# Kernel tuning notes

Measured on AMD Instinct MI355X. Metric: run time of the kernel, lower is better.

Reference implementation:

```python
import jax, jax.numpy as jnp
import numpy as np

DIM = 1024
HEADS = 16
DIM_HEAD = 64
INNER = HEADS * DIM_HEAD  # 1024
B, N = 4, 1024
SCALE = DIM_HEAD ** -0.5


def _layernorm(t, g, b, eps=1e-5):
    mu = jnp.mean(t, axis=-1, keepdims=True)
    var = jnp.var(t, axis=-1, keepdims=True)
    return (t - mu) * jax.lax.rsqrt(var + eps) * g + b


def setup_inputs() -> dict:
    key = jax.random.key(0)
    ks = jax.random.split(key, 8)
    return {
        "x": jax.random.normal(ks[0], (B, N, DIM), dtype=jnp.float32),
        "y": jax.random.normal(ks[1], (B, N, DIM), dtype=jnp.float32),
        "gx": jnp.ones((DIM,), jnp.float32),
        "bx": jnp.zeros((DIM,), jnp.float32),
        "gy": jnp.ones((DIM,), jnp.float32),
        "by": jnp.zeros((DIM,), jnp.float32),
        "Wqkv_x": jax.random.normal(ks[2], (DIM, 3 * INNER), jnp.float32) * 0.02,
        "Wqkv_y": jax.random.normal(ks[3], (DIM, 3 * INNER), jnp.float32) * 0.02,
        "Wout_x": jax.random.normal(ks[4], (INNER, DIM), jnp.float32) * 0.02,
        "bout_x": jnp.zeros((DIM,), jnp.float32),
        "Wout_y": jax.random.normal(ks[5], (INNER, DIM), jnp.float32) * 0.02,
        "bout_y": jnp.zeros((DIM,), jnp.float32),
    }


def _split_heads(t):
    b, n, _ = t.shape
    return t.reshape(b, n, HEADS, DIM_HEAD).transpose(0, 2, 1, 3)  # b h n d


def reference(x, y, gx, bx, gy, by, Wqkv_x, Wqkv_y, Wout_x, bout_x, Wout_y, bout_y):
    xn = _layernorm(x, gx, bx)
    yn = _layernorm(y, gy, by)
    qx, kx, vx = [_split_heads(t) for t in jnp.split(xn @ Wqkv_x, 3, axis=-1)]
    qy, ky, vy = [_split_heads(t) for t in jnp.split(yn @ Wqkv_y, 3, axis=-1)]
    # concat along HEADS dim -> 2h heads; each stream's heads attend within that stream
    q = jnp.concatenate([qx, qy], axis=1)
    k = jnp.concatenate([kx, ky], axis=1)
    v = jnp.concatenate([vx, vy], axis=1)
    dots = jnp.einsum('bhid,bhjd->bhij', q, k) * SCALE  # [B, 2h, N, N]
    attn = jax.nn.softmax(dots, axis=-1)
    out = jnp.einsum('bhij,bhjd->bhid', attn, v)  # [B, 2h, N, d]
    xo = out[:, :HEADS]  # original code uses the x-chunk for BOTH outputs (faithful)
    xo = xo.transpose(0, 2, 1, 3).reshape(xo.shape[0], xo.shape[2], INNER)  # b n (h d)
    out_x = xo @ Wout_x + bout_x
    out_y = xo @ Wout_y + bout_y
    return (out_x, out_y)
```

## Files before the change

### kernel.cpp

```cpp
#include <hip/hip_runtime.h>

typedef __attribute__((ext_vector_type(8))) short s16x8;
typedef __attribute__((ext_vector_type(4))) float f32x4;
typedef unsigned short u16;

#define DEV __device__ __forceinline__

DEV u16 f2bf(float f) {
    unsigned u = __builtin_bit_cast(unsigned, f);
    unsigned r = u + 0x7fffu + ((u >> 16) & 1u);
    return (u16)(r >> 16);
}

DEV float exp2a(float x) {
    float r;
    asm("v_exp_f32 %0, %1" : "=v"(r) : "v"(x));
    return r;
}

DEV unsigned cvtpk(float lo, float hi) {
    unsigned r;
    asm("v_cvt_pk_bf16_f32 %0, %1, %2" : "=v"(r) : "v"(lo), "v"(hi));
    return r;
}

DEV void gload_lds16(const void* g, void* l) {
    __builtin_amdgcn_global_load_lds(
        (const __attribute__((address_space(1))) unsigned int*)g,
        (__attribute__((address_space(3))) unsigned int*)l, 16, 0, 0);
}

DEV f32x4 mfma16(s16x8 a, s16x8 b, f32x4 c) {
    return __builtin_amdgcn_mfma_f32_16x16x32_bf16(a, b, c, 0, 0, 0);
}

template <int N>
DEV void vmwait() {
    asm volatile("s_waitcnt vmcnt(%0)" ::"n"(N) : "memory");
}

__global__ __launch_bounds__(256) void ln_kernel(const float* __restrict__ x,
                                                 const float* __restrict__ g,
                                                 const float* __restrict__ b,
                                                 u16* __restrict__ xn) {
    const int row = blockIdx.x, t = threadIdx.x;
    const float4 v = *(const float4*)(x + (size_t)row * 1024 + t * 4);
    float s1 = v.x + v.y + v.z + v.w;
    float s2 = v.x * v.x + v.y * v.y + v.z * v.z + v.w * v.w;
#pragma unroll
    for (int d = 1; d < 64; d <<= 1) {
        s1 += __shfl_xor(s1, d);
        s2 += __shfl_xor(s2, d);
    }
    __shared__ float red[8];
    if ((t & 63) == 0) { red[(t >> 6) * 2] = s1; red[(t >> 6) * 2 + 1] = s2; }
    __syncthreads();
    s1 = red[0] + red[2] + red[4] + red[6];
    s2 = red[1] + red[3] + red[5] + red[7];
    const float mu = s1 * (1.0f / 1024.0f);
    const float var = s2 * (1.0f / 1024.0f) - mu * mu;
    const float rs = rsqrtf(var + 1e-5f);
    const float4 gv = *(const float4*)(g + t * 4);
    const float4 bv = *(const float4*)(b + t * 4);
    ushort4 o;
    o.x = f2bf((v.x - mu) * rs * gv.x + bv.x);
    o.y = f2bf((v.y - mu) * rs * gv.y + bv.y);
    o.z = f2bf((v.z - mu) * rs * gv.z + bv.z);
    o.w = f2bf((v.w - mu) * rs * gv.w + bv.w);
    *(ushort4*)(xn + (size_t)row * 1024 + t * 4) = o;
}

__global__ __launch_bounds__(256) void transpose_w(const float* __restrict__ src,
                                                   u16* __restrict__ dst, int ld) {
    __shared__ float tile[64][68];
    const int t = threadIdx.x;
    const int n0 = blockIdx.x * 64, k0 = blockIdx.y * 64;
    const int kl = t >> 4, nl = (t & 15) * 4;
#pragma unroll
    for (int p = 0; p < 4; ++p) {
        float4 v = *(const float4*)(src + (size_t)(k0 + kl + p * 16) * ld + n0 + nl);
        tile[kl + p * 16][nl + 0] = v.x;
        tile[kl + p * 16][nl + 1] = v.y;
        tile[kl + p * 16][nl + 2] = v.z;
        tile[kl + p * 16][nl + 3] = v.w;
    }
    __syncthreads();
    const int nl2 = t >> 2, kc = (t & 3) * 16;
    __align__(16) u16 tmp[16];
#pragma unroll
    for (int j = 0; j < 16; ++j) tmp[j] = f2bf(tile[kc + j][nl2]);
    u16* d = dst + (size_t)(n0 + nl2) * 1024 + k0 + kc;
    ((uint4*)d)[0] = ((const uint4*)tmp)[0];
    ((uint4*)d)[1] = ((const uint4*)tmp)[1];
}

__global__ __launch_bounds__(256) void transpose_v(const u16* __restrict__ V,
                                                   u16* __restrict__ Vt) {
    __shared__ u16 tile[64][72];
    const int t = threadIdx.x;
    const int j0 = blockIdx.x * 64;
    const int bh = blockIdx.y;
    const u16* src = V + (size_t)bh * 65536;
    const int jl = t >> 4, dl = (t & 15) * 4;
#pragma unroll
    for (int p = 0; p < 4; ++p) {
        ushort4 v = *(const ushort4*)(src + (size_t)(j0 + jl + p * 16) * 64 + dl);
        *(ushort4*)&tile[jl + p * 16][dl] = v;
    }
    __syncthreads();
    const int dl2 = t >> 2, jc = (t & 3) * 16;
    __align__(16) u16 tmp[16];
#pragma unroll
    for (int j = 0; j < 16; ++j) tmp[j] = tile[jc + j][dl2];
    u16* d = Vt + (size_t)bh * 65536 + (size_t)dl2 * 1024 + j0 + jc;
    ((uint4*)d)[0] = ((const uint4*)tmp)[0];
    ((uint4*)d)[1] = ((const uint4*)tmp)[1];
}

template <int BN, int WM, int EPI>
__global__ __launch_bounds__(512, 2) void gemm8(const u16* __restrict__ A,
                                                const u16* __restrict__ B,
                                                u16* __restrict__ Qb, u16* __restrict__ Kb,
                                                u16* __restrict__ Vb,
                                                const float* __restrict__ bx,
                                                const float* __restrict__ by,
                                                float* __restrict__ out, int NBX) {
    constexpr int BM = 256, WN = 8 / WM;
    constexpr int TM = BM / WM, TN = BN / WN;
    constexpr int MQ = TM / 32, NQ = TN / 32;
    constexpr int HA = TM / 2, HB = TN / 2;
    constexpr int CHA = 1024;
    constexpr int CHB = BN * 4;
    constexpr int GA = 2, GB = CHB / 512;
    constexpr int NI = 8;

    __shared__ __align__(16) u16 As[2 * 2 * CHA * 8];
    __shared__ __align__(16) u16 Bs[2 * 2 * CHB * 8];

    const int tid = threadIdx.x, lane = tid & 63;
    const int wave = tid >> 6;
    const int wm = wave / WN, wn = wave % WN;
    const int lr = lane & 15, cg = lane >> 4;

    const int nwg = NBX * 16;
    const int bid = blockIdx.x;
    const int bid2 = (bid & 7) * (nwg >> 3) + (bid >> 3);
    const int bxi = bid2 % NBX, byi = bid2 / NBX;
    const int m0 = byi * 256, n0 = bxi * BN;

    const u16* __restrict__ Ag = A + (size_t)m0 * 1024;
    const u16* __restrict__ Bg = B + (size_t)n0 * 1024;

    f32x4 acc[2 * MQ][2 * NQ] = {};

#define STG_A(b, h, t)                                                              \
    do {                                                                            \
        _Pragma("unroll") for (int u = 0; u < GA; ++u) {                            \
            const int idx = u * 512 + tid;                                          \
            const int loc = idx >> 3, pp = idx & 7;                                 \
            const int row = (loc & (HA - 1)) | ((h)*HA) | ((loc / HA) * 2 * HA);    \
            gload_lds16(Ag + (size_t)row * 1024 + (t)*64 + ((pp ^ (row & 7)) << 3), \
                        &As[(((b)*2 + (h)) * CHA + idx) * 8]);                      \
        }                                                                           \
    } while (0)
#define STG_B(b, h, t)                                                              \
    do {                                                                            \
        _Pragma("unroll") for (int u = 0; u < GB; ++u) {                            \
            const int idx = u * 512 + tid;                                          \
            const int loc = idx >> 3, pp = idx & 7;                                 \
            const int row = (loc & (HB - 1)) | ((h)*HB) | ((loc / HB) * 2 * HB);    \
            gload_lds16(Bg + (size_t)row * 1024 + (t)*64 + ((pp ^ (row & 7)) << 3), \
                        &Bs[(((b)*2 + (h)) * CHB + idx) * 8]);                      \
        }                                                                           \
    } while (0)

#define LDA(bb, lm, dst)                                                            \
    _Pragma("unroll") for (int mf = 0; mf < MQ; ++mf)                               \
        _Pragma("unroll") for (int ks = 0; ks < 2; ++ks)                            \
            dst[mf][ks] = *(const s16x8*)&As[((((bb)*2 + (lm)) * CHA) +             \
                                              (mf * 16 + lr + wm * HA) * 8 +        \
                                              ((cg + ks * 4) ^ (lr & 7))) * 8];

#define LDB(bb, ln, dst)                                                            \
    _Pragma("unroll") for (int nf = 0; nf < NQ; ++nf)                               \
        _Pragma("unroll") for (int ks = 0; ks < 2; ++ks)                            \
            dst[nf][ks] = *(const s16x8*)&Bs[((((bb)*2 + (ln)) * CHB) +             \
                                              (nf * 16 + lr + wn * HB) * 8 +        \
                                              ((cg + ks * 4) ^ (lr & 7))) * 8];

#define MM(lm, ln, A_, B_)                                                          \
    __builtin_amdgcn_s_setprio(1);                                                  \
    _Pragma("unroll") for (int mf = 0; mf < MQ; ++mf)                               \
        _Pragma("unroll") for (int nf = 0; nf < NQ; ++nf)                           \
            _Pragma("unroll") for (int ks = 0; ks < 2; ++ks)                        \
                acc[(lm)*MQ + mf][(ln)*NQ + nf] = mfma16(                           \
                    A_[mf][ks], B_[nf][ks], acc[(lm)*MQ + mf][(ln)*NQ + nf]);       \
    __builtin_amdgcn_s_setprio(0);

#define BAR() asm volatile("s_barrier" ::: "memory")

    STG_A(0, 0, 0);
    STG_A(0, 1, 0);
    STG_B(0, 0, 0);
    STG_B(0, 1, 0);
    STG_A(1, 0, 1);
    STG_B(1, 0, 1);
    vmwait<GA + GB>();
    BAR();

    s16x8 va[MQ][2];
    s16x8 vb[2][NQ][2];

#pragma unroll 1
    for (int i = 0; i < NI - 1; ++i) {
        const int t1 = 2 * i + 1, t2 = 2 * i + 2, t3 = 2 * i + 3;
        LDA(0, 0, va); LDB(0, 0, vb[0]); STG_A(1, 1, t1); BAR(); MM(0, 0, va, vb[0]);
        LDB(0, 1, vb[1]);                STG_B(1, 1, t1); BAR(); MM(0, 1, va, vb[1]);
        LDA(0, 1, va);                   STG_A(0, 0, t2); BAR(); MM(1, 0, va, vb[0]);
        STG_B(0, 0, t2); vmwait<GA + GB>();               BAR(); MM(1, 1, va, vb[1]);
        LDA(1, 0, va); LDB(1, 0, vb[0]); STG_A(0, 1, t2); BAR(); MM(0, 0, va, vb[0]);
        LDB(1, 1, vb[1]);                STG_B(0, 1, t2); BAR(); MM(0, 1, va, vb[1]);
        LDA(1, 1, va);                   STG_A(1, 0, t3); BAR(); MM(1, 0, va, vb[0]);
        STG_B(1, 0, t3); vmwait<GA + GB>();               BAR(); MM(1, 1, va, vb[1]);
    }
    LDA(0, 0, va); LDB(0, 0, vb[0]); STG_A(1, 1, 15); BAR(); MM(0, 0, va, vb[0]);
    LDB(0, 1, vb[1]);                STG_B(1, 1, 15); BAR(); MM(0, 1, va, vb[1]);
    LDA(0, 1, va);                                    BAR(); MM(1, 0, va, vb[0]);
    vmwait<0>();                                      BAR(); MM(1, 1, va, vb[1]);
    LDA(1, 0, va); LDB(1, 0, vb[0]); MM(0, 0, va, vb[0]);
    LDB(1, 1, vb[1]);                MM(0, 1, va, vb[1]);
    LDA(1, 1, va);                   MM(1, 0, va, vb[0]);
    MM(1, 1, va, vb[1]);

#undef STG_A
#undef STG_B
#undef LDA
#undef LDB
#undef MM
#undef BAR

#pragma unroll
    for (int am = 0; am < 2 * MQ; ++am) {
        const int lm = am / MQ, mf = am % MQ;
        const int rowb = m0 + wm * TM + lm * HA + mf * 16 + cg * 4;
#pragma unroll
        for (int an = 0; an < 2 * NQ; ++an) {
            const int ln = an / NQ, nf = an % NQ;
            const int col = n0 + wn * TN + ln * HB + nf * 16 + lr;
            if (EPI == 0) {
                const int which = col >> 10, hd = col & 1023;
                const int h = hd >> 6, dd = hd & 63;
                u16* dst = (which == 0) ? Qb : (which == 1) ? Kb : Vb;
                const float sc = (which == 0) ? 0.18033688011112042f : 1.0f;
#pragma unroll
                for (int r = 0; r < 4; ++r) {
                    const int tk = rowb + r;
                    const int bb2 = tk >> 10, ii = tk & 1023;
                    dst[(size_t)(((bb2 << 4) + h) * 1024 + ii) * 64 + dd] =
                        f2bf(acc[am][an][r] * sc);
                }
            } else {
                float bias;
                float* ob;
                if (col < 1024) { bias = bx[col]; ob = out + col; }
                else { bias = by[col - 1024]; ob = out + 4194304 + (col - 1024); }
#pragma unroll
                for (int r = 0; r < 4; ++r)
                    ob[(size_t)(rowb + r) * 1024] = acc[am][an][r] + bias;
            }
        }
    }
}

__global__ __launch_bounds__(256) void attn_kernel(const u16* __restrict__ Q,
                                                   const u16* __restrict__ Kg,
                                                   const u16* __restrict__ Vt,
                                                   u16* __restrict__ xo) {
    __shared__ __align__(16) u16 Ks[2][64 * 64];
    __shared__ __align__(16) u16 Vs[2][64 * 64];
    __shared__ __align__(16) u16 Ps[4][32 * 64];
    const int tid = threadIdx.x, lane = tid & 63, w = tid >> 6;
    const int bh = blockIdx.x >> 3, qblk = blockIdx.x & 7;
    const u16* Qh = Q + (size_t)bh * 65536;
    const u16* Kh = Kg + (size_t)bh * 65536;
    const u16* Vh = Vt + (size_t)bh * 65536;
    const int lr = lane & 15, cg = lane >> 4;
    const int q0 = qblk * 128 + w * 32;
    u16* Pw = &Ps[w][0];

    s16x8 qf[2][2];
#pragma unroll
    for (int qg = 0; qg < 2; ++qg)
#pragma unroll
        for (int ks = 0; ks < 2; ++ks)
            qf[qg][ks] =
                *(const s16x8*)(Qh + (size_t)(q0 + qg * 16 + lr) * 64 + ks * 32 + cg * 8);

    f32x4 o[2][4] = {};
    float l_s[2] = {0.f, 0.f};
    float m_s[2] = {-3e38f, -3e38f};
    int ba[4];
#pragma unroll
    for (int r = 0; r < 4; ++r) ba[r] = (cg * 4 + r) * 4;

#define STAGEKV(bufi, kv0)                                                               \
    do {                                                                                 \
        _Pragma("unroll") for (int i = 0; i < 2; ++i) {                                  \
            int idx = i * 256 + tid;                                                     \
            int row = idx >> 3, p = idx & 7;                                             \
            gload_lds16(Kh + (size_t)((kv0) + row) * 64 + ((p ^ (row & 7)) << 3),        \
                        &Ks[bufi][idx * 8]);                                             \
            gload_lds16(Vh + (size_t)row * 1024 + (kv0) + ((p ^ (row & 7)) << 3),        \
                        &Vs[bufi][idx * 8]);                                             \
        }                                                                                \
    } while (0)

    STAGEKV(0, 0);
    asm volatile("s_waitcnt vmcnt(0)" ::: "memory");
    __syncthreads();

    for (int t = 0; t < 16; ++t) {
        const int buf = t & 1;
        if (t < 15) STAGEKV(buf ^ 1, (t + 1) * 64);

        f32x4 s[2][4] = {};
#pragma unroll
        for (int fn = 0; fn < 4; ++fn) {
            const int r = fn * 16 + lr;
#pragma unroll
            for (int ks = 0; ks < 2; ++ks) {
                const int c = cg + ks * 4;
                s16x8 kf = *(const s16x8*)&Ks[buf][r * 64 + ((c ^ (r & 7)) << 3)];
                s[0][fn] = mfma16(kf, qf[0][ks], s[0][fn]);
                s[1][fn] = mfma16(kf, qf[1][ks], s[1][fn]);
            }
        }

#pragma unroll
        for (int qg = 0; qg < 2; ++qg) {
            float tm = -3e38f;
#pragma unroll
            for (int fn = 0; fn < 4; ++fn)
#pragma unroll
                for (int r = 0; r < 4; ++r) tm = fmaxf(tm, s[qg][fn][r]);
            tm = fmaxf(tm, __shfl_xor(tm, 16));
            tm = fmaxf(tm, __shfl_xor(tm, 32));
            if (!__all(tm <= m_s[qg] + 8.0f)) {
                const float mn = fmaxf(m_s[qg], tm);
                const float corr = exp2a(m_s[qg] - mn);
                m_s[qg] = mn;
                l_s[qg] *= corr;
                f32x4 corr_o;
#pragma unroll
                for (int r = 0; r < 4; ++r)
                    corr_o[r] = __builtin_bit_cast(
                        float,
                        __builtin_amdgcn_ds_bpermute(ba[r], __builtin_bit_cast(int, corr)));
#pragma unroll
                for (int fd = 0; fd < 4; ++fd) o[qg][fd] *= corr_o;
            }
            const float mn = m_s[qg];
            float rs = 0.f;
            const int prow = (qg * 16 + lr) * 64;
#pragma unroll
            for (int fn = 0; fn < 4; ++fn) {
                const float p0 = exp2a(s[qg][fn][0] - mn);
                const float p1 = exp2a(s[qg][fn][1] - mn);
                const float p2 = exp2a(s[qg][fn][2] - mn);
                const float p3 = exp2a(s[qg][fn][3] - mn);
                rs += (p0 + p1) + (p2 + p3);
                uint2 dd;
                dd.x = cvtpk(p0, p1);
                dd.y = cvtpk(p2, p3);
                *(uint2*)(Pw + prow + (((2 * fn + (cg >> 1)) ^ (lr & 7)) << 3) +
                          ((cg & 1) << 2)) = dd;
            }
            rs += __shfl_xor(rs, 16);
            rs += __shfl_xor(rs, 32);
            l_s[qg] += rs;
        }

        s16x8 pf[2][2];
#pragma unroll
        for (int qg = 0; qg < 2; ++qg)
#pragma unroll
            for (int ks = 0; ks < 2; ++ks)
                pf[qg][ks] = *(const s16x8*)(Pw + (qg * 16 + lr) * 64 +
                                             (((4 * ks + cg) ^ (lr & 7)) << 3));
#pragma unroll
        for (int fd = 0; fd < 4; ++fd) {
            const int rr = fd * 16 + lr;
#pragma unroll
            for (int ks = 0; ks < 2; ++ks) {
                const int c = cg + ks * 4;
                s16x8 vf = *(const s16x8*)&Vs[buf][rr * 64 + ((c ^ (rr & 7)) << 3)];
                o[0][fd] = mfma16(pf[0][ks], vf, o[0][fd]);
                o[1][fd] = mfma16(pf[1][ks], vf, o[1][fd]);
            }
        }
        asm volatile("s_waitcnt vmcnt(0)" ::: "memory");
        __syncthreads();
    }
#undef STAGEKV

    const int b = bh >> 4, h = bh & 15;
#pragma unroll
    for (int qg = 0; qg < 2; ++qg) {
        f32x4 inv;
#pragma unroll
        for (int r = 0; r < 4; ++r) {
            const float lq = __builtin_bit_cast(
                float, __builtin_amdgcn_ds_bpermute(ba[r], __builtin_bit_cast(int, l_s[qg])));
            inv[r] = 1.0f / lq;
        }
#pragma unroll
        for (int r = 0; r < 4; ++r) {
            const int qrow = q0 + qg * 16 + cg * 4 + r;
#pragma unroll
            for (int fd = 0; fd < 4; ++fd)
                xo[(size_t)(b * 1024 + qrow) * 1024 + h * 64 + fd * 16 + lr] =
                    f2bf(o[qg][fd][r] * inv[r]);
        }
    }
}

extern "C" void kernel_launch(void* const* d_in, const int* in_sizes, int n_in,
                              void* d_out, int out_size, void* d_ws, size_t ws_size,
                              hipStream_t stream) {
    const float* x = (const float*)d_in[0];
    const float* gx = (const float*)d_in[2];
    const float* bxv = (const float*)d_in[3];
    const float* Wqkv = (const float*)d_in[6];
    const float* Woutx = (const float*)d_in[8];
    const float* boutx = (const float*)d_in[9];
    const float* Wouty = (const float*)d_in[10];
    const float* bouty = (const float*)d_in[11];
    float* out = (float*)d_out;

    u16* ws = (u16*)d_ws;
    u16* xn = ws;
    u16* wqkv_t = xn + 4096 * 1024;
    u16* wout_t = wqkv_t + 3072 * 1024;
    u16* Qb = wout_t + 2048 * 1024;
    u16* Kb = Qb + 64 * 1024 * 64;
    u16* Vb = Kb + 64 * 1024 * 64;
    u16* Vtb = Vb + 64 * 1024 * 64;
    u16* xob = Vtb + 64 * 1024 * 64;

    ln_kernel<<<4096, 256, 0, stream>>>(x, gx, bxv, xn);
    transpose_w<<<dim3(48, 16), 256, 0, stream>>>(Wqkv, wqkv_t, 3072);
    transpose_w<<<dim3(16, 16), 256, 0, stream>>>(Woutx, wout_t, 1024);
    transpose_w<<<dim3(16, 16), 256, 0, stream>>>(Wouty, wout_t + 1024 * 1024, 1024);
    gemm8<256, 2, 0><<<192, 512, 0, stream>>>(xn, wqkv_t, Qb, Kb, Vb, nullptr, nullptr,
                                              nullptr, 12);
    transpose_v<<<dim3(16, 64), 256, 0, stream>>>(Vb, Vtb);
    attn_kernel<<<512, 256, 0, stream>>>(Qb, Kb, Vtb, xob);
    gemm8<128, 4, 1><<<256, 512, 0, stream>>>(xob, wout_t, nullptr, nullptr, nullptr,
                                              boutx, bouty, out, 16);
}
```

Baseline: 119.3 us.

## Merge output-weight transposes into one launch and remap attention block order

The two output-projection weight transposes are combined into one launch, using blockIdx.z to pick the source matrix and destination slice, which removes one kernel launch. The attention kernel's block-to-(head, query-block) mapping is permuted so that consecutively numbered blocks cover different heads, which may change how work lands across compute dies and caches. The GEMM B-fragment register array is split into two named arrays, a cosmetic change that might alter register allocation. The extra launch removed is small, and the block remap could help or hurt cache locality.

```diff
diff --git a/kernel.cpp b/kernel.cpp
--- a/kernel.cpp
+++ b/kernel.cpp
@@ -70,10 +70,13 @@
     *(ushort4*)(xn + (size_t)row * 1024 + t * 4) = o;
 }
 
-__global__ __launch_bounds__(256) void transpose_w(const float* __restrict__ src,
+__global__ __launch_bounds__(256) void transpose_w(const float* __restrict__ src0,
+                                                   const float* __restrict__ src1,
                                                    u16* __restrict__ dst, int ld) {
     __shared__ float tile[64][68];
     const int t = threadIdx.x;
+    const float* src = (blockIdx.z == 0) ? src0 : src1;
+    u16* d0 = dst + (size_t)blockIdx.z * 1024 * 1024;
     const int n0 = blockIdx.x * 64, k0 = blockIdx.y * 64;
     const int kl = t >> 4, nl = (t & 15) * 4;
 #pragma unroll
@@ -89,7 +92,7 @@
     __align__(16) u16 tmp[16];
 #pragma unroll
     for (int j = 0; j < 16; ++j) tmp[j] = f2bf(tile[kc + j][nl2]);
-    u16* d = dst + (size_t)(n0 + nl2) * 1024 + k0 + kc;
+    u16* d = d0 + (size_t)(n0 + nl2) * 1024 + k0 + kc;
     ((uint4*)d)[0] = ((const uint4*)tmp)[0];
     ((uint4*)d)[1] = ((const uint4*)tmp)[1];
 }
@@ -209,28 +212,28 @@
     BAR();
 
     s16x8 va[MQ][2];
-    s16x8 vb[2][NQ][2];
+    s16x8 vb0[NQ][2], vb1[NQ][2];
 
 #pragma unroll 1
     for (int i = 0; i < NI - 1; ++i) {
         const int t1 = 2 * i + 1, t2 = 2 * i + 2, t3 = 2 * i + 3;
-        LDA(0, 0, va); LDB(0, 0, vb[0]); STG_A(1, 1, t1); BAR(); MM(0, 0, va, vb[0]);
-        LDB(0, 1, vb[1]);                STG_B(1, 1, t1); BAR(); MM(0, 1, va, vb[1]);
-        LDA(0, 1, va);                   STG_A(0, 0, t2); BAR(); MM(1, 0, va, vb[0]);
-        STG_B(0, 0, t2); vmwait<GA + GB>();               BAR(); MM(1, 1, va, vb[1]);
-        LDA(1, 0, va); LDB(1, 0, vb[0]); STG_A(0, 1, t2); BAR(); MM(0, 0, va, vb[0]);
-        LDB(1, 1, vb[1]);                STG_B(0, 1, t2); BAR(); MM(0, 1, va, vb[1]);
-        LDA(1, 1, va);                   STG_A(1, 0, t3); BAR(); MM(1, 0, va, vb[0]);
-        STG_B(1, 0, t3); vmwait<GA + GB>();               BAR(); MM(1, 1, va, vb[1]);
-    }
-    LDA(0, 0, va); LDB(0, 0, vb[0]); STG_A(1, 1, 15); BAR(); MM(0, 0, va, vb[0]);
-    LDB(0, 1, vb[1]);                STG_B(1, 1, 15); BAR(); MM(0, 1, va, vb[1]);
-    LDA(0, 1, va);                                    BAR(); MM(1, 0, va, vb[0]);
-    vmwait<0>();                                      BAR(); MM(1, 1, va, vb[1]);
-    LDA(1, 0, va); LDB(1, 0, vb[0]); MM(0, 0, va, vb[0]);
-    LDB(1, 1, vb[1]);                MM(0, 1, va, vb[1]);
-    LDA(1, 1, va);                   MM(1, 0, va, vb[0]);
-    MM(1, 1, va, vb[1]);
+        LDA(0, 0, va); LDB(0, 0, vb0); STG_A(1, 1, t1); BAR(); MM(0, 0, va, vb0);
+        LDB(0, 1, vb1);                STG_B(1, 1, t1); BAR(); MM(0, 1, va, vb1);
+        LDA(0, 1, va);                 STG_A(0, 0, t2); BAR(); MM(1, 0, va, vb0);
+        STG_B(0, 0, t2); vmwait<GA + GB>();             BAR(); MM(1, 1, va, vb1);
+        LDA(1, 0, va); LDB(1, 0, vb0); STG_A(0, 1, t2); BAR(); MM(0, 0, va, vb0);
+        LDB(1, 1, vb1);                STG_B(0, 1, t2); BAR(); MM(0, 1, va, vb1);
+        LDA(1, 1, va);                 STG_A(1, 0, t3); BAR(); MM(1, 0, va, vb0);
+        STG_B(1, 0, t3); vmwait<GA + GB>();             BAR(); MM(1, 1, va, vb1);
+    }
+    LDA(0, 0, va); LDB(0, 0, vb0); STG_A(1, 1, 15); BAR(); MM(0, 0, va, vb0);
+    LDB(0, 1, vb1);                STG_B(1, 1, 15); BAR(); MM(0, 1, va, vb1);
+    LDA(0, 1, va);                                  BAR(); MM(1, 0, va, vb0);
+    vmwait<0>();                                    BAR(); MM(1, 1, va, vb1);
+    LDA(1, 0, va); LDB(1, 0, vb0); MM(0, 0, va, vb0);
+    LDB(1, 1, vb1);                MM(0, 1, va, vb1);
+    LDA(1, 1, va);                 MM(1, 0, va, vb0);
+    MM(1, 1, va, vb1);
 
 #undef STG_A
 #undef STG_B
@@ -280,7 +283,9 @@
     __shared__ __align__(16) u16 Vs[2][64 * 64];
     __shared__ __align__(16) u16 Ps[4][32 * 64];
     const int tid = threadIdx.x, lane = tid & 63, w = tid >> 6;
-    const int bh = blockIdx.x >> 3, qblk = blockIdx.x & 7;
+    const int bid = blockIdx.x;
+    const int bh = (bid & 7) * 8 + ((bid >> 3) & 7);
+    const int qblk = bid >> 6;
     const u16* Qh = Q + (size_t)bh * 65536;
     const u16* Kh = Kg + (size_t)bh * 65536;
     const u16* Vh = Vt + (size_t)bh * 65536;
@@ -448,9 +453,8 @@
     u16* xob = Vtb + 64 * 1024 * 64;
 
     ln_kernel<<<4096, 256, 0, stream>>>(x, gx, bxv, xn);
-    transpose_w<<<dim3(48, 16), 256, 0, stream>>>(Wqkv, wqkv_t, 3072);
-    transpose_w<<<dim3(16, 16), 256, 0, stream>>>(Woutx, wout_t, 1024);
-    transpose_w<<<dim3(16, 16), 256, 0, stream>>>(Wouty, wout_t + 1024 * 1024, 1024);
+    transpose_w<<<dim3(48, 16, 1), 256, 0, stream>>>(Wqkv, nullptr, wqkv_t, 3072);
+    transpose_w<<<dim3(16, 16, 2), 256, 0, stream>>>(Woutx, Wouty, wout_t, 1024);
     gemm8<256, 2, 0><<<192, 512, 0, stream>>>(xn, wqkv_t, Qb, Kb, Vb, nullptr, nullptr,
                                               nullptr, 12);
     transpose_v<<<dim3(16, 64), 256, 0, stream>>>(Vb, Vtb);
```

After: 114.6 us. -3.9%, faster.
